# Performance work log

Hardware: AMD Instinct MI355X
Metric: run time of the kernel (lower is better)

The kernel has to match this reference:

```python
import jax, jax.numpy as jnp
import numpy as np

D_MODEL = 2048
NUM_Q_HEADS = 32
NUM_KV_HEADS = 8
HEAD_DIM = D_MODEL // NUM_Q_HEADS  # 64
NUM_GROUPS = NUM_Q_HEADS // NUM_KV_HEADS  # 4
SCALE = float(np.sqrt(HEAD_DIM))


def setup_inputs() -> dict:
    key = jax.random.key(0)
    ks = jax.random.split(key, 5)
    B, S = 2, 2048
    std = 1.0 / np.sqrt(D_MODEL)
    return {
        "x": jax.random.normal(ks[0], (B, S, D_MODEL), dtype=jnp.float32),
        "W_q": jax.random.normal(ks[1], (D_MODEL, NUM_Q_HEADS * HEAD_DIM), dtype=jnp.float32) * std,
        "W_k": jax.random.normal(ks[2], (D_MODEL, NUM_KV_HEADS * HEAD_DIM), dtype=jnp.float32) * std,
        "W_v": jax.random.normal(ks[3], (D_MODEL, NUM_KV_HEADS * HEAD_DIM), dtype=jnp.float32) * std,
        "W_o": jax.random.normal(ks[4], (D_MODEL, D_MODEL), dtype=jnp.float32) * std,
    }


def reference(x, W_q, W_k, W_v, W_o):
    B, S, _ = x.shape
    # projections; weights stored as (in, out) so y = x @ W
    Q = (x @ W_q).reshape(B, S, NUM_Q_HEADS, HEAD_DIM).transpose(0, 2, 1, 3)   # [B,Hq,S,d]
    K = (x @ W_k).reshape(B, S, NUM_KV_HEADS, HEAD_DIM).transpose(0, 2, 1, 3)  # [B,Hkv,S,d]
    V = (x @ W_v).reshape(B, S, NUM_KV_HEADS, HEAD_DIM).transpose(0, 2, 1, 3)
    # repeat_interleave KV heads across groups (faithful to the original)
    K = jnp.repeat(K, NUM_GROUPS, axis=1)  # [B,Hq,S,d]
    V = jnp.repeat(V, NUM_GROUPS, axis=1)
    scores = jnp.einsum("bhqd,bhkd->bhqk", Q, K) / SCALE  # [B,Hq,S,S]
    attn = jax.nn.softmax(scores, axis=-1)
    out = jnp.einsum("bhqk,bhkd->bhqd", attn, V)  # [B,Hq,S,d]
    out = out.transpose(0, 2, 1, 3).reshape(B, S, D_MODEL)
    return out @ W_o
```

## Files before the change

kernel.cpp:

```cpp
#include <hip/hip_runtime.h>
#include <hip/hip_bf16.h>

#define D_MODEL 2048
#define NQH 32
#define NKVH 8
#define HD 64
#define SEQ 2048
#define BATCH 2
#define MTOT (BATCH * SEQ)

typedef __attribute__((ext_vector_type(8))) short short8;
typedef __attribute__((ext_vector_type(4))) float floatx4;
typedef __attribute__((ext_vector_type(16))) float f32x16;

#define QSCALE 0.18033688011112042f

#if __has_builtin(__builtin_amdgcn_exp2f)
#define EXP2(x) __builtin_amdgcn_exp2f(x)
#else
static __device__ inline float vexp2(float x) {
  float r;
  asm("v_exp_f32 %0, %1\n\ts_nop 1" : "=v"(r) : "v"(x));
  return r;
}
#define EXP2(x) vexp2(x)
#endif

static __device__ inline unsigned cvtpk(float lo, float hi) {
  unsigned r;
  asm("v_cvt_pk_bf16_f32 %0, %1, %2" : "=v"(r) : "v"(lo), "v"(hi));
  return r;
}
#define PLSWAP(a, b) asm("v_permlane32_swap_b32 %0, %1" : "+v"(a), "+v"(b))

__device__ inline void gload_lds16(const __hip_bfloat16* g, short* lds) {
  __builtin_amdgcn_global_load_lds(
      (const __attribute__((address_space(1))) void*)g,
      (__attribute__((address_space(3))) void*)lds, 16, 0, 0);
}

__global__ __launch_bounds__(256) void prep_k(
    const float* __restrict__ Wq, const float* __restrict__ Wk,
    const float* __restrict__ Wv, const float* __restrict__ Wo,
    __hip_bfloat16* __restrict__ Wqt, __hip_bfloat16* __restrict__ Wkt,
    __hip_bfloat16* __restrict__ Wvt, __hip_bfloat16* __restrict__ Wot,
    const float* __restrict__ x, __hip_bfloat16* __restrict__ xb) {
  __shared__ float t[32][33];
  const int z = blockIdx.z;
  const int tx = threadIdx.x, ty = threadIdx.y;

  if (z == 4) {
    int flat = (blockIdx.y * 64 + blockIdx.x) * 256 + ty * 32 + tx;
#pragma unroll
    for (int rep = 0; rep < 2; ++rep) {
      int i = flat + rep * (64 * 64 * 256);
      float4 v = reinterpret_cast<const float4*>(x)[i];
      union { __hip_bfloat16 h[4]; uint2 u; } cv;
      cv.h[0] = __float2bfloat16(v.x);
      cv.h[1] = __float2bfloat16(v.y);
      cv.h[2] = __float2bfloat16(v.z);
      cv.h[3] = __float2bfloat16(v.w);
      reinterpret_cast<uint2*>(xb)[i] = cv.u;
    }
    return;
  }

  const int Nd = (z == 1 || z == 2) ? 512 : 2048;
  const int n0 = blockIdx.x * 32;
  if (n0 >= Nd) return;
  const float* W = (z == 0) ? Wq : (z == 1) ? Wk : (z == 2) ? Wv : Wo;
  __hip_bfloat16* Wt = (z == 0) ? Wqt : (z == 1) ? Wkt : (z == 2) ? Wvt : Wot;
  const int Kd = D_MODEL;
  const int k0 = blockIdx.y * 32;
#pragma unroll
  for (int j = 0; j < 32; j += 8)
    t[ty + j][tx] = W[(size_t)(k0 + ty + j) * Nd + n0 + tx];
  __syncthreads();
#pragma unroll
  for (int j = 0; j < 32; j += 8)
    Wt[(size_t)(n0 + ty + j) * Kd + k0 + tx] = __float2bfloat16(t[tx][ty + j]);
}

__global__ __launch_bounds__(512, 1) void gemmqkv_k(
    const __hip_bfloat16* __restrict__ A,
    const __hip_bfloat16* __restrict__ B0,
    const __hip_bfloat16* __restrict__ B1,
    const __hip_bfloat16* __restrict__ B2,
    __hip_bfloat16* __restrict__ O0,
    __hip_bfloat16* __restrict__ O1,
    __hip_bfloat16* __restrict__ O2) {
  constexpr int Kd = D_MODEL;
  constexpr int NT = Kd / 64;

  __shared__ short Asb[2][16384];
  __shared__ short Bsb[3][12288];

  const int bid = blockIdx.x;
  const int swz = (bid & 7) * 32 + (bid >> 3);
  const int by = swz >> 4, bx = swz & 15;
  const int m0 = by * 256, n0 = bx * 192;

  const __hip_bfloat16* Ab = A + (size_t)m0 * Kd;

  const __hip_bfloat16* bp[3];
#pragma unroll
  for (int L = 0; L < 3; ++L) {
    int nr = n0 + L * 64;
    bp[L] = (nr < 2048) ? B0 + (size_t)nr * Kd
          : (nr < 2560) ? B1 + (size_t)(nr - 2048) * Kd
                        : B2 + (size_t)(nr - 2560) * Kd;
  }

  const int tid = threadIdx.x, w = tid >> 6, l = tid & 63;
  const int wm = w >> 1, wn = w & 1;
  const int lc = l & 15, l4 = l >> 4;

  const int srow = w * 8 + (l >> 3);
  const int scc = (l & 7) ^ ((l >> 3) & 7);

#define STAGE_A(L, SB, KT) \
  gload_lds16(Ab + (size_t)((L)*64 + srow) * Kd + (KT) + scc * 8, &Asb[SB][(L)*4096 + w * 512])
#define STAGE_B(L, SB, KT) \
  gload_lds16(bp[L] + (size_t)srow * Kd + (KT) + scc * 8, &Bsb[SB][(L)*4096 + w * 512])

  floatx4 acc[4][6] = {};

  int cx[2];
#pragma unroll
  for (int kk = 0; kk < 2; ++kk) cx[kk] = (((kk * 4 + l4) ^ (lc & 7)) * 8);
  const int abase = (wm * 64 + lc) * 64;
  const int bbase = (wn * 96 + lc) * 64;

  STAGE_A(0, 0, 0); STAGE_A(1, 0, 0); STAGE_A(2, 0, 0); STAGE_A(3, 0, 0);
  STAGE_B(0, 0, 0); STAGE_B(1, 0, 0); STAGE_B(2, 0, 0);
  STAGE_B(0, 1, 64); STAGE_B(1, 1, 64); STAGE_B(2, 1, 64);
  asm volatile("s_waitcnt vmcnt(3)" ::: "memory");
  __builtin_amdgcn_s_barrier();

  short8 af[4], bfr[6];

  for (int t = 0; t < NT; ++t) {
    const short* Ar = Asb[t & 1];
    const short* Br = Bsb[t % 3];

    if (t + 1 < NT) {
      const int kt = (t + 1) * 64, sa = (t + 1) & 1;
      STAGE_A(0, sa, kt); STAGE_A(1, sa, kt); STAGE_A(2, sa, kt); STAGE_A(3, sa, kt);
    }
    if (t + 2 < NT) {
      const int kt = (t + 2) * 64, sb = (t + 2) % 3;
      STAGE_B(0, sb, kt); STAGE_B(1, sb, kt); STAGE_B(2, sb, kt);
    }

#pragma unroll
    for (int kk = 0; kk < 2; ++kk) {
#pragma unroll
      for (int mi = 0; mi < 4; ++mi)
        af[mi] = *reinterpret_cast<const short8*>(&Ar[abase + mi * 1024 + cx[kk]]);
#pragma unroll
      for (int ni = 0; ni < 6; ++ni)
        bfr[ni] = *reinterpret_cast<const short8*>(&Br[bbase + ni * 1024 + cx[kk]]);
      __builtin_amdgcn_s_setprio(1);
#pragma unroll
      for (int mi = 0; mi < 4; ++mi)
#pragma unroll
        for (int ni = 0; ni < 6; ++ni)
          acc[mi][ni] = __builtin_amdgcn_mfma_f32_16x16x32_bf16(
              af[mi], bfr[ni], acc[mi][ni], 0, 0, 0);
      __builtin_amdgcn_s_setprio(0);
    }

    if (t < NT - 2)
      asm volatile("s_waitcnt vmcnt(3)" ::: "memory");
    else
      asm volatile("s_waitcnt vmcnt(0)" ::: "memory");
    __builtin_amdgcn_s_barrier();
  }
#undef STAGE_A
#undef STAGE_B

#pragma unroll
  for (int mi = 0; mi < 4; ++mi)
#pragma unroll
    for (int ni = 0; ni < 6; ++ni)
#pragma unroll
      for (int i = 0; i < 4; ++i) {
        int m = m0 + wm * 64 + mi * 16 + l4 * 4 + i;
        int ncol = n0 + wn * 96 + ni * 16 + lc;
        float v = acc[mi][ni][i];
        int bb = m >> 11, s = m & 2047;
        if (ncol < 2048) {
          int hh = ncol >> 6, dd = ncol & 63;
          O0[(((size_t)bb * NQH + hh) * SEQ + s) * HD + dd] = __float2bfloat16(v * QSCALE);
        } else if (ncol < 2560) {
          int c2 = ncol - 2048;
          int hh = c2 >> 6, dd = c2 & 63;
          O1[(((size_t)bb * NKVH + hh) * SEQ + s) * HD + dd] = __float2bfloat16(v);
        } else {
          int c2 = ncol - 2560;
          int hh = c2 >> 6, dd = c2 & 63;
          O2[(((size_t)bb * NKVH + hh) * HD + dd) * SEQ + s] = __float2bfloat16(v);
        }
      }
}

__global__ __launch_bounds__(512, 1) void gemmo_k(
    const __hip_bfloat16* __restrict__ A,
    const __hip_bfloat16* __restrict__ B0,
    float* __restrict__ Cf) {
  constexpr int Kd = D_MODEL;
  constexpr int NT = Kd / 64;
  constexpr int NB = 16;
  constexpr int NWG = 16 * NB;

  __shared__ short Asb[3][16384];
  __shared__ short Bsb[3][8192];

  const int bid = blockIdx.x;
  const int swz = (bid & 7) * (NWG / 8) + (bid >> 3);
  const int by = swz / NB, bx = swz % NB;
  const int m0 = by * 256, n0 = bx * 128;

  const __hip_bfloat16* Bt = B0 + (size_t)n0 * Kd;
  const __hip_bfloat16* Ab = A + (size_t)m0 * Kd;

  const int tid = threadIdx.x, w = tid >> 6, l = tid & 63;
  const int wm = w >> 1, wn = w & 1;
  const int lc = l & 15, l4 = l >> 4;

  const int srow = w * 8 + (l >> 3);
  const int scc = (l & 7) ^ ((l >> 3) & 7);

#define STAGE_A(L, SB, KT) \
  gload_lds16(Ab + (size_t)((L)*64 + srow) * Kd + (KT) + scc * 8, &Asb[SB][(L)*4096 + w * 512])
#define STAGE_B(L, SB, KT) \
  gload_lds16(Bt + (size_t)((L)*64 + srow) * Kd + (KT) + scc * 8, &Bsb[SB][(L)*4096 + w * 512])

  floatx4 acc[4][4] = {};

  int cx[2];
#pragma unroll
  for (int kk = 0; kk < 2; ++kk) cx[kk] = (((kk * 4 + l4) ^ (lc & 7)) * 8);
  const int abase = (wm * 64 + lc) * 64;
  const int bbase = (wn * 64 + lc) * 64;

  STAGE_A(0, 0, 0); STAGE_A(1, 0, 0); STAGE_A(2, 0, 0); STAGE_A(3, 0, 0);
  STAGE_B(0, 0, 0); STAGE_B(1, 0, 0);
  STAGE_A(0, 1, 64); STAGE_A(1, 1, 64); STAGE_A(2, 1, 64); STAGE_A(3, 1, 64);
  STAGE_B(0, 1, 64); STAGE_B(1, 1, 64);
  asm volatile("s_waitcnt vmcnt(6)" ::: "memory");
  __builtin_amdgcn_s_barrier();

  short8 af[4], bfr[4];

  for (int t = 0; t < NT; ++t) {
    const int rb = t % 3, sb = (t + 2) % 3;
    const int ksrc = ((t + 2) % NT) * 64;
    const short* Ar = Asb[rb];
    const short* Br = Bsb[rb];

#pragma unroll
    for (int mi = 0; mi < 4; ++mi)
      af[mi] = *reinterpret_cast<const short8*>(&Ar[abase + mi * 1024 + cx[0]]);
#pragma unroll
    for (int ni = 0; ni < 4; ++ni)
      bfr[ni] = *reinterpret_cast<const short8*>(&Br[bbase + ni * 1024 + cx[0]]);

    STAGE_A(0, sb, ksrc); STAGE_A(1, sb, ksrc); STAGE_B(0, sb, ksrc);

    __builtin_amdgcn_s_barrier();
    asm volatile("s_waitcnt lgkmcnt(0)" ::: "memory");
    __builtin_amdgcn_sched_barrier(0);
    __builtin_amdgcn_s_setprio(1);
#pragma unroll
    for (int mi = 0; mi < 4; ++mi)
#pragma unroll
      for (int ni = 0; ni < 4; ++ni)
        acc[mi][ni] = __builtin_amdgcn_mfma_f32_16x16x32_bf16(
            af[mi], bfr[ni], acc[mi][ni], 0, 0, 0);
    __builtin_amdgcn_s_setprio(0);
    __builtin_amdgcn_s_barrier();

#pragma unroll
    for (int mi = 0; mi < 4; ++mi)
      af[mi] = *reinterpret_cast<const short8*>(&Ar[abase + mi * 1024 + cx[1]]);
#pragma unroll
    for (int ni = 0; ni < 4; ++ni)
      bfr[ni] = *reinterpret_cast<const short8*>(&Br[bbase + ni * 1024 + cx[1]]);

    STAGE_A(2, sb, ksrc); STAGE_A(3, sb, ksrc); STAGE_B(1, sb, ksrc);

    asm volatile("s_waitcnt vmcnt(6)" ::: "memory");
    __builtin_amdgcn_s_barrier();
    asm volatile("s_waitcnt lgkmcnt(0)" ::: "memory");
    __builtin_amdgcn_sched_barrier(0);
    __builtin_amdgcn_s_setprio(1);
#pragma unroll
    for (int mi = 0; mi < 4; ++mi)
#pragma unroll
      for (int ni = 0; ni < 4; ++ni)
        acc[mi][ni] = __builtin_amdgcn_mfma_f32_16x16x32_bf16(
            af[mi], bfr[ni], acc[mi][ni], 0, 0, 0);
    __builtin_amdgcn_s_setprio(0);
    __builtin_amdgcn_s_barrier();
  }
#undef STAGE_A
#undef STAGE_B

#pragma unroll
  for (int mi = 0; mi < 4; ++mi)
#pragma unroll
    for (int ni = 0; ni < 4; ++ni)
#pragma unroll
      for (int i = 0; i < 4; ++i) {
        int m = m0 + wm * 64 + mi * 16 + l4 * 4 + i;
        int ncol = n0 + wn * 64 + ni * 16 + lc;
        Cf[(size_t)m * 2048 + ncol] = acc[mi][ni][i];
      }
}

__global__ __launch_bounds__(256, 4) void attn_k(const __hip_bfloat16* __restrict__ Qb,
                                                 const __hip_bfloat16* __restrict__ Kb,
                                                 const __hip_bfloat16* __restrict__ Vtb,
                                                 __hip_bfloat16* __restrict__ Ao) {
  __shared__ short Ks[2][64 * 64];
  __shared__ short Vs[2][64 * 64];

  const int bid = blockIdx.x;
  const int xcd = bid & 7, j = bid >> 3;
  const int g = xcd * 2 + (j >> 6), wv = j & 63;
  const int b = g >> 3, kh = g & 7;
  const int h = kh * 4 + (wv >> 4), qt = wv & 15;

  const int tid = threadIdx.x, w = tid >> 6, l = tid & 63;
  const int q5 = l & 31, hl = l >> 5;

  const __hip_bfloat16* Qp = Qb + (((size_t)b * NQH + h) * SEQ + qt * 128 + w * 32) * HD;
  const __hip_bfloat16* Kp = Kb + ((size_t)b * NKVH + kh) * SEQ * HD;
  const __hip_bfloat16* Vp = Vtb + ((size_t)b * NKVH + kh) * HD * SEQ;

  short8 qf[4];
#pragma unroll
  for (int ks = 0; ks < 4; ++ks)
    qf[ks] = *reinterpret_cast<const short8*>(Qp + (size_t)q5 * HD + ks * 16 + hl * 8);

  f32x16 acc0 = {}, acc1 = {};
  float lsum = 0.f;

  const int rg = l >> 3;
  const int cc = (l & 7) ^ (rg & 7);
  const __hip_bfloat16* sK = Kp + (size_t)(16 * w + rg) * HD + cc * 8;
  const __hip_bfloat16* sV = Vp + (size_t)(16 * w + rg) * SEQ + cc * 8;

  int fo[4];
#pragma unroll
  for (int jj = 0; jj < 4; ++jj)
    fo[jj] = q5 * 64 + (((jj * 2 + hl) ^ (q5 & 7)) * 8);

  gload_lds16(sK, &Ks[0][1024 * w]);
  gload_lds16(sK + 8 * HD, &Ks[0][1024 * w + 512]);
  gload_lds16(sV, &Vs[0][1024 * w]);
  gload_lds16(sV + 8 * (size_t)SEQ, &Vs[0][1024 * w + 512]);
  sK += 64 * HD;
  sV += 64;
  __syncthreads();

  for (int kb = 0; kb < SEQ / 64; ++kb) {
    const short* Kt = Ks[kb & 1];
    const short* Vt = Vs[kb & 1];

    if (kb + 1 < SEQ / 64) {
      short* Kn = Ks[(kb & 1) ^ 1];
      short* Vn = Vs[(kb & 1) ^ 1];
      gload_lds16(sK, &Kn[1024 * w]);
      gload_lds16(sK + 8 * HD, &Kn[1024 * w + 512]);
      gload_lds16(sV, &Vn[1024 * w]);
      gload_lds16(sV + 8 * (size_t)SEQ, &Vn[1024 * w + 512]);
      sK += 64 * HD;
      sV += 64;
    }

    short8 kf0[4], kf1[4];
#pragma unroll
    for (int ks = 0; ks < 4; ++ks) {
      kf0[ks] = *reinterpret_cast<const short8*>(&Kt[fo[ks]]);
      kf1[ks] = *reinterpret_cast<const short8*>(&Kt[fo[ks] + 2048]);
    }
    f32x16 st0 = {}, st1 = {};
    __builtin_amdgcn_s_setprio(1);
#pragma unroll
    for (int ks = 0; ks < 4; ++ks) {
      st0 = __builtin_amdgcn_mfma_f32_32x32x16_bf16(kf0[ks], qf[ks], st0, 0, 0, 0);
      st1 = __builtin_amdgcn_mfma_f32_32x32x16_bf16(kf1[ks], qf[ks], st1, 0, 0, 0);
    }
    __builtin_amdgcn_s_setprio(0);

    float ps = 0.f;
    unsigned u0[8], u1[8];
#pragma unroll
    for (int jj = 0; jj < 8; ++jj) {
      float e0 = EXP2(st0[2 * jj]), e1 = EXP2(st0[2 * jj + 1]);
      float f0 = EXP2(st1[2 * jj]), f1 = EXP2(st1[2 * jj + 1]);
      ps += (e0 + e1) + (f0 + f1);
      u0[jj] = cvtpk(e0, e1);
      u1[jj] = cvtpk(f0, f1);
    }
    lsum += ps;

    short8 vf0[4], vf1[4];
#pragma unroll
    for (int t = 0; t < 4; ++t) {
      vf0[t] = *reinterpret_cast<const short8*>(&Vt[fo[t]]);
      vf1[t] = *reinterpret_cast<const short8*>(&Vt[fo[t] + 2048]);
    }

    PLSWAP(u0[0], u0[2]); PLSWAP(u0[1], u0[3]);
    PLSWAP(u0[4], u0[6]); PLSWAP(u0[5], u0[7]);
    PLSWAP(u1[0], u1[2]); PLSWAP(u1[1], u1[3]);
    PLSWAP(u1[4], u1[6]); PLSWAP(u1[5], u1[7]);

    __builtin_amdgcn_s_setprio(1);
#pragma unroll
    for (int t = 0; t < 4; ++t) {
      union { unsigned w4[4]; short8 s8; } pa;
      pa.w4[0] = (t >> 1 ? u1 : u0)[(t & 1) * 4 + 0];
      pa.w4[1] = (t >> 1 ? u1 : u0)[(t & 1) * 4 + 1];
      pa.w4[2] = (t >> 1 ? u1 : u0)[(t & 1) * 4 + 2];
      pa.w4[3] = (t >> 1 ? u1 : u0)[(t & 1) * 4 + 3];
      acc0 = __builtin_amdgcn_mfma_f32_32x32x16_bf16(pa.s8, vf0[t], acc0, 0, 0, 0);
      acc1 = __builtin_amdgcn_mfma_f32_32x32x16_bf16(pa.s8, vf1[t], acc1, 0, 0, 0);
    }
    __builtin_amdgcn_s_setprio(0);
    __syncthreads();
  }

  float* Ls = reinterpret_cast<float*>(&Ks[0][0]);
  {
    float v = lsum;
    v += __shfl_xor(v, 32);
    if (l < 32) Ls[w * 32 + l] = v;
  }
  __syncthreads();

  const size_t obase = (size_t)b * SEQ + qt * 128 + w * 32;
  float inv[16];
#pragma unroll
  for (int r = 0; r < 16; ++r)
    inv[r] = 1.0f / Ls[w * 32 + (r & 3) + 8 * (r >> 2) + 4 * hl];
#pragma unroll
  for (int r = 0; r < 16; ++r) {
    int q = (r & 3) + 8 * (r >> 2) + 4 * hl;
    Ao[(obase + q) * D_MODEL + h * HD + q5] = __float2bfloat16(acc0[r] * inv[r]);
    Ao[(obase + q) * D_MODEL + h * HD + 32 + q5] = __float2bfloat16(acc1[r] * inv[r]);
  }
}

extern "C" void kernel_launch(void* const* d_in, const int* in_sizes, int n_in,
                              void* d_out, int out_size, void* d_ws, size_t ws_size,
                              hipStream_t stream) {
  const float* x  = (const float*)d_in[0];
  const float* Wq = (const float*)d_in[1];
  const float* Wk = (const float*)d_in[2];
  const float* Wv = (const float*)d_in[3];
  const float* Wo = (const float*)d_in[4];
  float* out = (float*)d_out;

  __hip_bfloat16* p = (__hip_bfloat16*)d_ws;
  __hip_bfloat16* xb  = p;
  __hip_bfloat16* Wqt = xb  + (size_t)MTOT * D_MODEL;
  __hip_bfloat16* Wkt = Wqt + (size_t)D_MODEL * D_MODEL;
  __hip_bfloat16* Wvt = Wkt + (size_t)512 * D_MODEL;
  __hip_bfloat16* Wot = Wvt + (size_t)512 * D_MODEL;
  __hip_bfloat16* Qb  = Wot + (size_t)D_MODEL * D_MODEL;
  __hip_bfloat16* Kb  = Qb  + (size_t)MTOT * D_MODEL;
  __hip_bfloat16* Vtb = Kb  + (size_t)BATCH * NKVH * SEQ * HD;
  __hip_bfloat16* Ab  = Vtb + (size_t)BATCH * NKVH * SEQ * HD;

  prep_k<<<dim3(64, 64, 5), dim3(32, 8), 0, stream>>>(Wq, Wk, Wv, Wo,
                                                      Wqt, Wkt, Wvt, Wot, x, xb);

  gemmqkv_k<<<dim3(256), 512, 0, stream>>>(xb, Wqt, Wkt, Wvt, Qb, Kb, Vtb);
  attn_k<<<dim3(1024), 256, 0, stream>>>(Qb, Kb, Vtb, Ab);
  gemmo_k<<<dim3(256), 512, 0, stream>>>(Ab, Wot, out);
}
```

Before: 216.7 us.

## Triple-buffer K/V tiles in attention kernel with partial vmcnt waits

Attention kernel moves from double to triple buffering of K/V LDS tiles, prefetching two blocks ahead. Full __syncthreads is replaced by s_waitcnt vmcnt(4) plus a barrier, so one block's loads can stay in flight across iterations and load latency is hidden better. LDS use rises to 48KB per block and launch bounds drop to 3 blocks per CU, which may reduce occupancy.

```diff
diff --git a/kernel.cpp b/kernel.cpp
--- a/kernel.cpp
+++ b/kernel.cpp
@@ -319,12 +319,12 @@
       }
 }
 
-__global__ __launch_bounds__(256, 4) void attn_k(const __hip_bfloat16* __restrict__ Qb,
+__global__ __launch_bounds__(256, 3) void attn_k(const __hip_bfloat16* __restrict__ Qb,
                                                  const __hip_bfloat16* __restrict__ Kb,
                                                  const __hip_bfloat16* __restrict__ Vtb,
                                                  __hip_bfloat16* __restrict__ Ao) {
-  __shared__ short Ks[2][64 * 64];
-  __shared__ short Vs[2][64 * 64];
+  __shared__ short KsA[3][4096];
+  __shared__ short VsA[3][4096];
 
   const int bid = blockIdx.x;
   const int xcd = bid & 7, j = bid >> 3;
@@ -357,28 +357,31 @@
   for (int jj = 0; jj < 4; ++jj)
     fo[jj] = q5 * 64 + (((jj * 2 + hl) ^ (q5 & 7)) * 8);
 
-  gload_lds16(sK, &Ks[0][1024 * w]);
-  gload_lds16(sK + 8 * HD, &Ks[0][1024 * w + 512]);
-  gload_lds16(sV, &Vs[0][1024 * w]);
-  gload_lds16(sV + 8 * (size_t)SEQ, &Vs[0][1024 * w + 512]);
-  sK += 64 * HD;
-  sV += 64;
-  __syncthreads();
-
+#define STG(DSTK, DSTV)                                   \
+  do {                                                    \
+    gload_lds16(sK, (DSTK) + 1024 * w);                   \
+    gload_lds16(sK + 8 * HD, (DSTK) + 1024 * w + 512);    \
+    gload_lds16(sV, (DSTV) + 1024 * w);                   \
+    gload_lds16(sV + 8 * (size_t)SEQ, (DSTV) + 1024 * w + 512); \
+    sK += 64 * HD;                                        \
+    sV += 64;                                             \
+  } while (0)
+
+  STG(&KsA[0][0], &VsA[0][0]);
+  STG(&KsA[1][0], &VsA[1][0]);
+  asm volatile("s_waitcnt vmcnt(4)" ::: "memory");
+  __builtin_amdgcn_s_barrier();
+
+  int rb = 0, sb = 2;
   for (int kb = 0; kb < SEQ / 64; ++kb) {
-    const short* Kt = Ks[kb & 1];
-    const short* Vt = Vs[kb & 1];
-
-    if (kb + 1 < SEQ / 64) {
-      short* Kn = Ks[(kb & 1) ^ 1];
-      short* Vn = Vs[(kb & 1) ^ 1];
-      gload_lds16(sK, &Kn[1024 * w]);
-      gload_lds16(sK + 8 * HD, &Kn[1024 * w + 512]);
-      gload_lds16(sV, &Vn[1024 * w]);
-      gload_lds16(sV + 8 * (size_t)SEQ, &Vn[1024 * w + 512]);
-      sK += 64 * HD;
-      sV += 64;
-    }
+    if (kb + 2 < SEQ / 64) {
+      short* Kd = &KsA[0][0] + sb * 4096;
+      short* Vd = &VsA[0][0] + sb * 4096;
+      STG(Kd, Vd);
+    }
+
+    const short* Kt = &KsA[0][0] + rb * 4096;
+    const short* Vt = &VsA[0][0] + rb * 4096;
 
     short8 kf0[4], kf1[4];
 #pragma unroll
@@ -431,10 +434,21 @@
       acc1 = __builtin_amdgcn_mfma_f32_32x32x16_bf16(pa.s8, vf1[t], acc1, 0, 0, 0);
     }
     __builtin_amdgcn_s_setprio(0);
-    __syncthreads();
-  }
-
-  float* Ls = reinterpret_cast<float*>(&Ks[0][0]);
+
+    if (kb < SEQ / 64 - 1) {
+      if (kb <= SEQ / 64 - 3)
+        asm volatile("s_waitcnt vmcnt(4)" ::: "memory");
+      else
+        asm volatile("s_waitcnt vmcnt(0)" ::: "memory");
+      __builtin_amdgcn_s_barrier();
+    }
+    rb = (rb == 2) ? 0 : rb + 1;
+    sb = (sb == 2) ? 0 : sb + 1;
+  }
+#undef STG
+
+  __syncthreads();
+  float* Ls = reinterpret_cast<float*>(&KsA[0][0]);
   {
     float v = lsum;
     v += __shfl_xor(v, 32);
```

Measured after the change: 215.6 us. No clear change (-0.5%).
